# Optimization experiments

Measured on AMD Instinct MI355X. Metric: run time of the kernel, lower is better.

Reference implementation:

```python
import jax, jax.numpy as jnp
import numpy as np

D = 11          # tree depth (root level); leaves at depth 0
B = 16          # trees per batch
D_MODEL = 256   # params.emb_dim
VOCAB = 512     # len(id2word)


def _build_forest():
    """B perfect binary trees, nodes laid out level-by-level (leaves first)."""
    widths = [2 ** (D - k) for k in range(D + 1)]          # nodes per level
    off = np.concatenate([[0], np.cumsum(widths)]).astype(np.int64)
    per = int(off[-1])                                      # 2^(D+1)-1 = 4095
    depths_t = np.concatenate([np.full(w, k, np.int64) for k, w in enumerate(widths)])
    left_t = np.zeros(per, np.int64)
    right_t = np.zeros(per, np.int64)
    for k in range(1, D + 1):
        loc = np.arange(widths[k])
        idx = off[k] + loc
        left_t[idx] = off[k - 1] + 2 * loc
        right_t[idx] = off[k - 1] + 2 * loc + 1
    toff = (np.arange(B) * per)[:, None]                    # global node offsets per tree
    depths = np.tile(depths_t, B)
    left = (left_t[None, :] + toff).reshape(-1)
    right = (right_t[None, :] + toff).reshape(-1)
    leaf_ids = (np.arange(widths[0])[None, :] + toff).reshape(-1)
    internal = np.concatenate([
        (off[k] + np.arange(widths[k])[None, :] + toff).reshape(-1)
        for k in range(1, D + 1)
    ])                                                      # sorted by depth ascending
    return depths, left, right, leaf_ids, internal, per


def setup_inputs() -> dict:
    key = jax.random.key(0)
    k1, k2, k3 = jax.random.split(key, 3)
    depths, left, right, leaf_ids, internal, per = _build_forest()
    N = B * per
    tokens = jax.random.randint(k1, (N,), 0, VOCAB, dtype=jnp.int32)
    # learned params: leaf embedding table (max_norm=1.0 semantics), TreeLSTM cell
    emb = jax.random.normal(k2, (VOCAB, D_MODEL), dtype=jnp.float32) * 0.02
    W = jax.random.normal(k3, (2 * D_MODEL, 5 * D_MODEL), dtype=jnp.float32) / np.sqrt(2.0 * D_MODEL)
    b = jnp.zeros((5 * D_MODEL,), jnp.float32)
    operation_order = jnp.concatenate([jnp.array([-1], jnp.int32), jnp.full((D,), 7, jnp.int32)])
    lengths = jnp.full((B,), per, dtype=jnp.int32)
    return {
        "tokens": tokens,
        "left_idx": jnp.asarray(left, jnp.int32),
        "right_idx": jnp.asarray(right, jnp.int32),
        "depths": jnp.asarray(depths, jnp.int32),
        "operation_order": operation_order,
        "lengths": lengths,
        "leaf_ids": jnp.asarray(leaf_ids, jnp.int32),
        "internal_ids": jnp.asarray(internal, jnp.int32),
        "emb": emb,
        "W": W,
        "b": b,
    }


def _leaf_embed(emb, toks):
    # torch Embedding(max_norm=1.0): rows renormalized to L2 norm <= 1 at lookup
    e = emb[toks]
    nrm = jnp.linalg.norm(e, axis=-1, keepdims=True)
    return e * jnp.minimum(1.0, 1.0 / jnp.maximum(nrm, 1e-7))


def reference(tokens, left_idx, right_idx, depths, operation_order, lengths,
              leaf_ids, internal_ids, emb, W, b):
    N = tokens.shape[0]
    d = emb.shape[1]
    num_steps = operation_order.shape[0]   # = D + 1
    depth = num_steps - 1
    batch = lengths.shape[0]

    # step 0: leaves (operation_order[0] == -1) -> masked_scatter of embeddings
    acts = jnp.zeros((N, d), dtype=emb.dtype).at[leaf_ids].add(_leaf_embed(emb, tokens[leaf_ids]))
    mem = jnp.zeros((N, d), dtype=emb.dtype)   # memory_size = 1, cell state per node

    start = 0
    for k in range(1, depth + 1):
        width = batch * (2 ** (depth - k))      # static per-depth node count
        ids = internal_ids[start:start + width]
        start += width
        li = left_idx[ids]
        ri = right_idx[ids]
        hl, hr = acts[li], acts[ri]             # gather child activations [w, d]
        cl, cr = mem[li], mem[ri]               # gather child cell states [w, d]
        # binary N-ary TreeLSTM cell (_apply_function)
        g = jnp.concatenate([hl, hr], axis=-1) @ W + b   # [w, 5d]
        i, fl, fr, o, u = jnp.split(g, 5, axis=-1)
        c = jax.nn.sigmoid(i) * jnp.tanh(u) + jax.nn.sigmoid(fl) * cl + jax.nn.sigmoid(fr) * cr
        h = jax.nn.sigmoid(o) * jnp.tanh(c)
        # torch_scatter.scatter(...) added onto running buffers
        acts = acts.at[ids].add(h)
        mem = mem.at[ids].add(c)

    # _compute_output: split by equal lengths + pad_sequence -> [B, per_tree, d]
    return acts.reshape(batch, -1, d)
```

## Files before the change

kernel.cpp:

```cpp
#include <hip/hip_runtime.h>
#include <stdint.h>

using bf16   = __bf16;
using bf16x4 = __attribute__((ext_vector_type(4))) __bf16;
using bf16x8 = __attribute__((ext_vector_type(8))) __bf16;
using f32x4  = __attribute__((ext_vector_type(4))) float;

#define DEPTH   11
#define NTREES  16
#define DM      256
#define PER     4095
#define KDIM    512
#define NGATES  5

__device__ __forceinline__ float sigf(float x) { return 1.0f / (1.0f + __expf(-x)); }
__device__ __forceinline__ float tanh_fast(float x) {
    float e = __expf(2.0f * x);
    return 1.0f - 2.0f / (e + 1.0f);
}

__device__ __forceinline__ void load_lds16(const bf16* g, bf16* l) {
    __builtin_amdgcn_global_load_lds((const __attribute__((address_space(1))) void*)g,
                                     (__attribute__((address_space(3))) void*)l,
                                     16, 0, 0);
}

__global__ __launch_bounds__(256) void setup_kernel(
        const float* __restrict__ W, bf16* __restrict__ Wf,
        const int* __restrict__ tokens, const float* __restrict__ emb,
        float* acts, bf16* actsb) {
    int bid = blockIdx.x;
    if (bid < 320) {
        int tid = bid * 256 + threadIdx.x;
        int f   = tid >> 6;
        int l   = tid & 63;
        int gt  = f >> 4;
        int ks  = f & 15;
        int n   = (gt << 4) + (l & 15);
        int k0  = (ks << 5) + ((l >> 4) << 3);
        bf16x8 v;
        #pragma unroll
        for (int e = 0; e < 8; ++e) v[e] = (bf16)W[(size_t)(k0 + e) * 1280 + n];
        *reinterpret_cast<bf16x8*>(Wf + (size_t)tid * 8) = v;
        return;
    }
    int wid  = ((bid - 320) * 256 + threadIdx.x) >> 6;
    int lane = threadIdx.x & 63;
    int b    = wid >> 11;
    int loc  = wid & 2047;
    int id   = b * PER + loc;
    int tok  = tokens[id];

    float4 e = *reinterpret_cast<const float4*>(emb + tok * DM + lane * 4);
    float ss = e.x * e.x + e.y * e.y + e.z * e.z + e.w * e.w;
    #pragma unroll
    for (int off = 32; off; off >>= 1) ss += __shfl_xor(ss, off);
    float scale = fminf(1.0f, 1.0f / fmaxf(sqrtf(ss), 1e-7f));
    e.x *= scale; e.y *= scale; e.z *= scale; e.w *= scale;

    int o = id * DM + lane * 4;
    *reinterpret_cast<float4*>(acts + o) = e;
    bf16x4 eb;
    eb.x = (bf16)e.x; eb.y = (bf16)e.y; eb.z = (bf16)e.z; eb.w = (bf16)e.w;
    *reinterpret_cast<bf16x4*>(actsb + o) = eb;
}

__global__ __launch_bounds__(256, 2) void level_big(
        const bf16* __restrict__ actsb_in, const bf16* __restrict__ Wfrag,
        const float* __restrict__ bias, float* __restrict__ mem,
        float* __restrict__ acts, bf16* __restrict__ actsb_out,
        int off_k, int off_km1, int zmem) {
    constexpr int RPB = 64;
    constexpr int NRG = 4;
    constexpr int NLD = 4;
    __shared__ __align__(16) bf16 ldsA[2][16][RPB][8];

    int t    = threadIdx.x;
    int lane = t & 63;
    int w    = t >> 6;
    int lo   = lane & 15;
    int hi   = lane >> 4;

    int rt    = blockIdx.x >> 2;
    int uct   = blockIdx.x & 3;
    int b     = blockIdx.y;
    int rm    = rt * RPB;
    int wslot = (uct << 2) + w;

    const bf16* Abase = actsb_in + (size_t)(b * PER + off_km1) * DM;

    const bf16* aSrc[NLD];
    #pragma unroll
    for (int i = 0; i < NLD; ++i) {
        int s   = i * 256 + t;
        aSrc[i] = Abase + (size_t)(rm + (s & (RPB - 1))) * KDIM + (s / RPB) * 8;
    }

    const bf16* bbase = Wfrag + ((size_t)wslot << 13) + lane * 8;

    int ucol = (wslot << 4) + lo;
    float bi[NGATES];
    #pragma unroll
    for (int g = 0; g < NGATES; ++g) bi[g] = bias[g * DM + ucol];

    #pragma unroll
    for (int i = 0; i < NLD; ++i)
        load_lds16(aSrc[i], &ldsA[0][0][0][0] + (i * 256 + t) * 8);

    f32x4 acc[NGATES][NRG] = {};

    __syncthreads();

    for (int kt = 0; kt < 4; ++kt) {
        int cur = kt & 1;
        if (kt < 3) {
            int ko = (kt + 1) * 128;
            #pragma unroll
            for (int i = 0; i < NLD; ++i)
                load_lds16(aSrc[i] + ko, &ldsA[cur ^ 1][0][0][0] + (i * 256 + t) * 8);
        }

        #pragma unroll
        for (int kq = 0; kq < 4; ++kq) {
            bf16x8 bb[NGATES];
            #pragma unroll
            for (int g = 0; g < NGATES; ++g)
                bb[g] = *reinterpret_cast<const bf16x8*>(bbase + (size_t)(((g << 8) | ((kt << 2) + kq)) << 9));
            #pragma unroll
            for (int rg = 0; rg < NRG; ++rg) {
                bf16x8 af = *reinterpret_cast<const bf16x8*>(&ldsA[cur][(kq << 2) + hi][(rg << 4) + lo][0]);
                #pragma unroll
                for (int g = 0; g < NGATES; ++g)
                    acc[g][rg] = __builtin_amdgcn_mfma_f32_16x16x32_bf16(af, bb[g], acc[g][rg], 0, 0, 0);
            }
        }
        __syncthreads();
    }

    int treebase = b * PER;
    #pragma unroll
    for (int rg = 0; rg < NRG; ++rg) {
        #pragma unroll
        for (int r = 0; r < 4; ++r) {
            int ml = rm + (rg << 4) + (hi << 2) + r;
            int id = treebase + off_k + ml;
            float cl = 0.0f, cr = 0.0f;
            if (!zmem) {
                int ch = (treebase + off_km1 + (ml << 1)) * DM + ucol;
                cl = mem[ch];
                cr = mem[ch + DM];
            }
            float gi = acc[0][rg][r] + bi[0];
            float gl = acc[1][rg][r] + bi[1];
            float gr = acc[2][rg][r] + bi[2];
            float go = acc[3][rg][r] + bi[3];
            float gu = acc[4][rg][r] + bi[4];
            float c  = sigf(gi) * tanh_fast(gu) + sigf(gl) * cl + sigf(gr) * cr;
            float h  = sigf(go) * tanh_fast(c);
            int oi = id * DM + ucol;
            acts[oi]      = h;
            mem[oi]       = c;
            actsb_out[oi] = (bf16)h;
        }
    }
}

__global__ __launch_bounds__(512) void level_splitk(
        const bf16* __restrict__ actsb_in, const bf16* __restrict__ Wfrag,
        const float* __restrict__ bias, float* mem, float* acts, bf16* actsb_out,
        int off_k, int off_km1, int shift) {
    __shared__ f32x4 red[7][NGATES][64];

    int t    = threadIdx.x;
    int lane = t & 63;
    int w    = t >> 6;
    int lo   = lane & 15;
    int hi   = lane >> 4;
    int tile = blockIdx.x >> 4;
    int uc   = blockIdx.x & 15;
    int m0   = tile << 4;
    int mask = (1 << shift) - 1;

    int mA   = m0 + lo;
    int rowA = (mA >> shift) * PER + off_km1 + ((mA & mask) << 1);
    const bf16* aptr  = actsb_in + (size_t)rowA * DM + hi * 8 + (w << 1) * 32;
    const bf16* bbase = Wfrag + ((size_t)uc << 13) + lane * 8;

    f32x4 acc[NGATES] = {};
    #pragma unroll
    for (int kk = 0; kk < 2; ++kk) {
        int kt = (w << 1) + kk;
        bf16x8 a = *reinterpret_cast<const bf16x8*>(aptr + kk * 32);
        #pragma unroll
        for (int g = 0; g < NGATES; ++g) {
            bf16x8 bb = *reinterpret_cast<const bf16x8*>(bbase + (size_t)(((g << 8) + kt) << 9));
            acc[g] = __builtin_amdgcn_mfma_f32_16x16x32_bf16(a, bb, acc[g], 0, 0, 0);
        }
    }

    if (w) {
        #pragma unroll
        for (int g = 0; g < NGATES; ++g) red[w - 1][g][lane] = acc[g];
    }
    __syncthreads();
    if (w == 0) {
        int ucol = (uc << 4) + lo;
        float bi[NGATES];
        #pragma unroll
        for (int g = 0; g < NGATES; ++g) {
            #pragma unroll
            for (int p = 0; p < 7; ++p) acc[g] += red[p][g][lane];
            bi[g] = bias[g * DM + ucol];
        }
        #pragma unroll
        for (int r = 0; r < 4; ++r) {
            int m   = m0 + (hi << 2) + r;
            int tb  = (m >> shift) * PER;
            int loc = m & mask;
            int id  = tb + off_k + loc;
            int ch  = (tb + off_km1 + (loc << 1)) * DM + ucol;
            float cl = mem[ch];
            float cr = mem[ch + DM];
            float gi = acc[0][r] + bi[0];
            float gl = acc[1][r] + bi[1];
            float gr = acc[2][r] + bi[2];
            float go = acc[3][r] + bi[3];
            float gu = acc[4][r] + bi[4];
            float c  = sigf(gi) * tanh_fast(gu) + sigf(gl) * cl + sigf(gr) * cr;
            float h  = sigf(go) * tanh_fast(c);
            int oi = id * DM + ucol;
            acts[oi]      = h;
            mem[oi]       = c;
            actsb_out[oi] = (bf16)h;
        }
    }
}

extern "C" void kernel_launch(void* const* d_in, const int* in_sizes, int n_in,
                              void* d_out, int out_size, void* d_ws, size_t ws_size,
                              hipStream_t stream) {
    (void)in_sizes; (void)n_in; (void)out_size; (void)ws_size;
    const int*   tokens = (const int*)d_in[0];
    const float* emb    = (const float*)d_in[8];
    const float* W      = (const float*)d_in[9];
    const float* bias   = (const float*)d_in[10];
    float* acts = (float*)d_out;

    char* ws = (char*)d_ws;
    bf16*  Wfrag = (bf16*)ws;
    bf16*  actsb = (bf16*)(ws + 1310720);
    float* mem   = (float*)(ws + 1310720 + 33546240);

    setup_kernel<<<dim3(320 + 8192), dim3(256), 0, stream>>>(
        W, Wfrag, tokens, emb, acts, actsb);

    int off_km1 = 0;
    for (int k = 1; k <= DEPTH; ++k) {
        int shift   = DEPTH - k;
        int Mt      = 1 << shift;
        int off_k   = off_km1 + (Mt << 1);
        int M_total = NTREES << shift;
        if (Mt >= 128) {
            level_big<<<dim3((Mt / 64) * 4, NTREES), dim3(256), 0, stream>>>(
                actsb, Wfrag, bias, mem, acts, actsb, off_k, off_km1, (k == 1) ? 1 : 0);
        } else {
            level_splitk<<<dim3(M_total), dim3(512), 0, stream>>>(
                actsb, Wfrag, bias, mem, acts, actsb, off_k, off_km1, shift);
        }
        off_km1 = off_k;
    }
}
```

Measured before the change: 168.4 us.

## Add 128-row 8-wave GEMM kernel with transposed bf16 weights for wide levels

Adds a setup stage that writes a K-contiguous transposed bf16 copy of W. It also adds a new level kernel using 512 threads and 128-row tiles, with double-buffered LDS staging of both A and B via global_load_lds and an XOR swizzle on B. This kernel handles the widest tree levels (Mt >= 512), so each block reuses weights across more rows and has more waves to hide latency. The cost is extra setup work, a larger workspace, and one block per CU with large LDS use.

```diff
diff --git a/kernel.cpp b/kernel.cpp
--- a/kernel.cpp
+++ b/kernel.cpp
@@ -26,7 +26,7 @@
 }
 
 __global__ __launch_bounds__(256) void setup_kernel(
-        const float* __restrict__ W, bf16* __restrict__ Wf,
+        const float* __restrict__ W, bf16* __restrict__ Wf, bf16* __restrict__ Wt,
         const int* __restrict__ tokens, const float* __restrict__ emb,
         float* acts, bf16* actsb) {
     int bid = blockIdx.x;
@@ -44,7 +44,29 @@
         *reinterpret_cast<bf16x8*>(Wf + (size_t)tid * 8) = v;
         return;
     }
-    int wid  = ((bid - 320) * 256 + threadIdx.x) >> 6;
+    if (bid < 480) {
+        __shared__ float tile[64][65];
+        int t  = threadIdx.x;
+        int bb = bid - 320;
+        int kt = bb / 20;
+        int nt = bb - kt * 20;
+        int kk0 = kt << 6, n0 = nt << 6;
+        int rr = t >> 6;
+        int cc = t & 63;
+        #pragma unroll
+        for (int i = 0; i < 16; ++i) {
+            int kl = (rr << 4) + i;
+            tile[kl][cc] = W[(size_t)(kk0 + kl) * 1280 + n0 + cc];
+        }
+        __syncthreads();
+        #pragma unroll
+        for (int i = 0; i < 16; ++i) {
+            int nl = (rr << 4) + i;
+            Wt[(size_t)(n0 + nl) * KDIM + kk0 + cc] = (bf16)tile[cc][nl];
+        }
+        return;
+    }
+    int wid  = ((bid - 480) * 256 + threadIdx.x) >> 6;
     int lane = threadIdx.x & 63;
     int b    = wid >> 11;
     int loc  = wid & 2047;
@@ -63,6 +85,126 @@
     bf16x4 eb;
     eb.x = (bf16)e.x; eb.y = (bf16)e.y; eb.z = (bf16)e.z; eb.w = (bf16)e.w;
     *reinterpret_cast<bf16x4*>(actsb + o) = eb;
+}
+
+__global__ __launch_bounds__(512, 1) void level_8p(
+        const bf16* __restrict__ actsb_in, const bf16* __restrict__ Wt,
+        const float* __restrict__ bias, float* __restrict__ mem,
+        float* __restrict__ acts, bf16* __restrict__ actsb_out,
+        int off_k, int off_km1, int zmem) {
+    __shared__ __align__(16) bf16 ldsA[2][8][128][8];
+    __shared__ __align__(16) bf16 ldsB[2][320][8][8];
+
+    int t    = threadIdx.x;
+    int lane = t & 63;
+    int w    = t >> 6;
+    int lo   = lane & 15;
+    int hi   = lane >> 4;
+    int rw   = w >> 2;
+    int uw   = w & 3;
+
+    int rt  = blockIdx.x >> 2;
+    int uct = blockIdx.x & 3;
+    int b   = blockIdx.y;
+    int rm  = rt << 7;
+    int uc0 = uct << 6;
+
+    const bf16* Abase = actsb_in + (size_t)(b * PER + off_km1) * DM;
+
+    const bf16* aSrc[2];
+    #pragma unroll
+    for (int i = 0; i < 2; ++i) {
+        int s   = i * 512 + t;
+        aSrc[i] = Abase + (size_t)(rm + (s & 127)) * KDIM + (s >> 7) * 8;
+    }
+    const bf16* bSrc[5];
+    #pragma unroll
+    for (int j = 0; j < 5; ++j) {
+        int s   = j * 512 + t;
+        int cc  = s >> 3;
+        int kb  = (s & 7) ^ (cc & 7);
+        int n   = (cc >> 6) * DM + uc0 + (cc & 63);
+        bSrc[j] = Wt + (size_t)n * KDIM + kb * 8;
+    }
+
+    int ucol = uc0 + (uw << 4) + lo;
+    float bi[NGATES];
+    #pragma unroll
+    for (int g = 0; g < NGATES; ++g) bi[g] = bias[g * DM + ucol];
+
+    #pragma unroll
+    for (int i = 0; i < 2; ++i)
+        load_lds16(aSrc[i], &ldsA[0][0][0][0] + (i * 512 + t) * 8);
+    #pragma unroll
+    for (int j = 0; j < 5; ++j)
+        load_lds16(bSrc[j], &ldsB[0][0][0][0] + (j * 512 + t) * 8);
+
+    f32x4 acc[NGATES][4] = {};
+
+    __syncthreads();
+
+    for (int kt = 0; kt < 8; ++kt) {
+        int cur = kt & 1;
+        bf16* dstA = &ldsA[cur ^ 1][0][0][0];
+        bf16* dstB = &ldsB[cur ^ 1][0][0][0];
+        int ko = (kt + 1) * 64;
+
+        #pragma unroll
+        for (int kq = 0; kq < 2; ++kq) {
+            if (kt < 7 && kq == 0) {
+                load_lds16(aSrc[0] + ko, dstA + t * 8);
+                load_lds16(aSrc[1] + ko, dstA + (512 + t) * 8);
+                #pragma unroll
+                for (int j = 0; j < 5; ++j)
+                    load_lds16(bSrc[j] + ko, dstB + (j * 512 + t) * 8);
+            }
+
+            bf16x8 bb[NGATES];
+            #pragma unroll
+            for (int g = 0; g < NGATES; ++g) {
+                int cc  = (g << 6) + (uw << 4) + lo;
+                int kbp = ((kq << 2) + hi) ^ (cc & 7);
+                bb[g] = *reinterpret_cast<const bf16x8*>(&ldsB[cur][cc][kbp][0]);
+            }
+            #pragma unroll
+            for (int rg = 0; rg < 4; ++rg) {
+                bf16x8 af = *reinterpret_cast<const bf16x8*>(
+                    &ldsA[cur][(kq << 2) + hi][(rw << 6) + (rg << 4) + lo][0]);
+                #pragma unroll
+                for (int g = 0; g < NGATES; ++g)
+                    acc[g][rg] = __builtin_amdgcn_mfma_f32_16x16x32_bf16(af, bb[g], acc[g][rg], 0, 0, 0);
+            }
+            if (kq == 0) __builtin_amdgcn_s_barrier();
+        }
+        __syncthreads();
+    }
+
+    int treebase = b * PER;
+    #pragma unroll
+    for (int rg = 0; rg < 4; ++rg) {
+        #pragma unroll
+        for (int r = 0; r < 4; ++r) {
+            int ml = rm + (rw << 6) + (rg << 4) + (hi << 2) + r;
+            int id = treebase + off_k + ml;
+            float cl = 0.0f, cr = 0.0f;
+            if (!zmem) {
+                int ch = (treebase + off_km1 + (ml << 1)) * DM + ucol;
+                cl = mem[ch];
+                cr = mem[ch + DM];
+            }
+            float gi = acc[0][rg][r] + bi[0];
+            float gl = acc[1][rg][r] + bi[1];
+            float gr = acc[2][rg][r] + bi[2];
+            float go = acc[3][rg][r] + bi[3];
+            float gu = acc[4][rg][r] + bi[4];
+            float c  = sigf(gi) * tanh_fast(gu) + sigf(gl) * cl + sigf(gr) * cr;
+            float h  = sigf(go) * tanh_fast(c);
+            int oi = id * DM + ucol;
+            acts[oi]      = h;
+            mem[oi]       = c;
+            actsb_out[oi] = (bf16)h;
+        }
+    }
 }
 
 __global__ __launch_bounds__(256, 2) void level_big(
@@ -248,11 +390,12 @@
 
     char* ws = (char*)d_ws;
     bf16*  Wfrag = (bf16*)ws;
-    bf16*  actsb = (bf16*)(ws + 1310720);
-    float* mem   = (float*)(ws + 1310720 + 33546240);
-
-    setup_kernel<<<dim3(320 + 8192), dim3(256), 0, stream>>>(
-        W, Wfrag, tokens, emb, acts, actsb);
+    bf16*  Wt    = (bf16*)(ws + 1310720);
+    bf16*  actsb = (bf16*)(ws + 2621440);
+    float* mem   = (float*)(ws + 2621440 + 33546240);
+
+    setup_kernel<<<dim3(480 + 8192), dim3(256), 0, stream>>>(
+        W, Wfrag, Wt, tokens, emb, acts, actsb);
 
     int off_km1 = 0;
     for (int k = 1; k <= DEPTH; ++k) {
@@ -260,9 +403,12 @@
         int Mt      = 1 << shift;
         int off_k   = off_km1 + (Mt << 1);
         int M_total = NTREES << shift;
-        if (Mt >= 128) {
+        if (Mt >= 512) {
+            level_8p<<<dim3((Mt >> 7) * 4, NTREES), dim3(512), 0, stream>>>(
+                actsb, Wt, bias, mem, acts, actsb, off_k, off_km1, (k == 1) ? 1 : 0);
+        } else if (Mt >= 128) {
             level_big<<<dim3((Mt / 64) * 4, NTREES), dim3(256), 0, stream>>>(
-                actsb, Wfrag, bias, mem, acts, actsb, off_k, off_km1, (k == 1) ? 1 : 0);
+                actsb, Wfrag, bias, mem, acts, actsb, off_k, off_km1, 0);
         } else {
             level_splitk<<<dim3(M_total), dim3(512), 0, stream>>>(
                 actsb, Wfrag, bias, mem, acts, actsb, off_k, off_km1, shift);
```

After: 169.3 us. No clear change (+0.5%).
